# Kernel optimization log

Hardware: AMD Instinct MI355X
Metric: run time of the kernel (lower is better)

The kernel has to match this reference:

```python
import jax, jax.numpy as jnp
import numpy as np

T, B, IN, H = 256, 64, 512, 1024

def setup_inputs() -> dict:
    key = jax.random.key(0)
    ks = jax.random.split(key, 8)
    s_in = 1.0 / np.sqrt(IN)
    s_h = 1.0 / np.sqrt(H)
    return {
        "inp": jax.random.normal(ks[0], (T, B, IN), jnp.float32),
        "img": jax.random.normal(ks[1], (B, H), jnp.float32),
        "Wxh": jax.random.uniform(ks[2], (4 * H, IN), jnp.float32, -s_in, s_in),
        "bxh": jax.random.uniform(ks[3], (4 * H,), jnp.float32, -s_in, s_in),
        "Whh": jax.random.uniform(ks[4], (4 * H, H), jnp.float32, -s_h, s_h),
        "bhh": jax.random.uniform(ks[5], (4 * H,), jnp.float32, -s_h, s_h),
        "Wout": jax.random.uniform(ks[6], (IN, H), jnp.float32, -s_h, s_h),
        "bout": jax.random.uniform(ks[7], (IN,), jnp.float32, -s_h, s_h),
    }

def reference(inp, img, Wxh, bxh, Whh, bhh, Wout, bout):
    t_len, b, _ = inp.shape
    h_dim = Whh.shape[1]
    img4 = jnp.concatenate([img, img, img, img], axis=1)  # [B, 4H]
    # precompute input projection for all timesteps: [T, B, 4H]
    xproj = jnp.einsum('tbi,gi->tbg', inp, Wxh) + bxh
    xproj = xproj.at[0].add(img4)

    def step(carry, xg):
        h, c = carry
        gates = xg + h @ Whh.T + bhh  # [B, 4H]
        i_g, f_g, g_g, o_g = jnp.split(gates, 4, axis=1)
        c = jax.nn.sigmoid(f_g) * c + jax.nn.sigmoid(i_g) * jnp.tanh(g_g)
        h = jax.nn.sigmoid(o_g) * jnp.tanh(c)
        return (h, c), h

    zeros = jnp.zeros((b, h_dim), inp.dtype)
    _, hs = jax.lax.scan(step, (zeros, zeros), xproj)  # hs: [T, B, H]
    out = jnp.einsum('tbh,vh->tbv', hs, Wout) + bout  # [T, B, IN]
    return jax.nn.log_softmax(out, axis=-1)
```

## Files before the change

kernel.cpp:

```cpp
#include <hip/hip_runtime.h>
#include <math.h>

#define T_LEN 256
#define B_SZ  64
#define IN_D  512
#define H_D   1024
#define G4    4096

typedef float  f32x4 __attribute__((ext_vector_type(4)));
typedef short  s16x8 __attribute__((ext_vector_type(8)));
typedef unsigned int u32x4 __attribute__((ext_vector_type(4)));
typedef unsigned short u16;
typedef unsigned int   u32;

__device__ __forceinline__ void gl_lds16(const void* g, void* l) {
  __builtin_amdgcn_global_load_lds(
      (const __attribute__((address_space(1))) unsigned int*)g,
      (__attribute__((address_space(3))) unsigned int*)l, 16, 0, 0);
}

__device__ __forceinline__ u16 f2bf(float f) {
  union { float f; unsigned u; } v; v.f = f;
  unsigned x = v.u;
  unsigned r = (x + 0x7fffu + ((x >> 16) & 1u)) >> 16;
  return (u16)r;
}
__device__ __forceinline__ float bf2f(u16 b) {
  union { unsigned u; float f; } v; v.u = ((unsigned)b) << 16;
  return v.f;
}
__device__ __forceinline__ float sigm(float x) {
  return 1.0f / (1.0f + __expf(-x));
}
__device__ __forceinline__ float tanh_f(float x) {
  float e = __expf(2.0f * x);
  return 1.0f - 2.0f / (e + 1.0f);
}

__global__ void cvt_f32_bf16(const float* __restrict__ src, u16* __restrict__ dst, int n) {
  int i = blockIdx.x * blockDim.x + threadIdx.x;
  int stride = gridDim.x * blockDim.x;
  for (; i < n; i += stride) dst[i] = f2bf(src[i]);
}

__global__ void fill_sentinel(u32* __restrict__ p, int n4) {
  int i = blockIdx.x * blockDim.x + threadIdx.x;
  int stride = gridDim.x * blockDim.x;
  u32x4 s = {0xFFFFFFFFu, 0xFFFFFFFFu, 0xFFFFFFFFu, 0xFFFFFFFFu};
  for (; i < n4; i += stride) {
    u32* dst = p + (size_t)i * 4;
    asm volatile("global_store_dwordx4 %0, %1, off sc1" :: "v"(dst), "v"(s) : "memory");
  }
}

template<int KD, int EPI>
__launch_bounds__(256)
__global__ void gemm_bt(const u16* __restrict__ A, const u16* __restrict__ Bm,
                        const float* __restrict__ bias, const float* __restrict__ img,
                        u16* __restrict__ Cb, float* __restrict__ Cf, int Ncols) {
  __shared__ u16 sA[128 * 64];
  __shared__ u16 sB[128 * 64];
  const int tid  = threadIdx.x;
  const int wave = tid >> 6, lane = tid & 63;
  const int wm = wave >> 1, wn = wave & 1;
  const int mBase = blockIdx.y * 128;
  const int nBase = blockIdx.x * 128;

  f32x4 acc[4][4] = {};

  for (int k0 = 0; k0 < KD; k0 += 64) {
#pragma unroll
    for (int it = 0; it < 4; ++it) {
      int s = it * 256 + tid;
      int row = s >> 3, c = s & 7;
      int gc = c ^ (row & 7);
      const u16* ga = A  + (size_t)(mBase + row) * KD + k0 + gc * 8;
      const u16* gb = Bm + (size_t)(nBase + row) * KD + k0 + gc * 8;
      gl_lds16(ga, &sA[(it * 256 + wave * 64) * 8]);
      gl_lds16(gb, &sB[(it * 256 + wave * 64) * 8]);
    }
    __syncthreads();

    const int q = lane >> 4, rl = lane & 15;
#pragma unroll
    for (int ks = 0; ks < 64; ks += 32) {
      s16x8 af[4], bfr[4];
      int gcb = (ks >> 3) + q;
#pragma unroll
      for (int i = 0; i < 4; ++i) {
        int rowA = wm * 64 + i * 16 + rl;
        af[i]  = *(const s16x8*)&sA[rowA * 64 + (gcb ^ (rowA & 7)) * 8];
        int rowB = wn * 64 + i * 16 + rl;
        bfr[i] = *(const s16x8*)&sB[rowB * 64 + (gcb ^ (rowB & 7)) * 8];
      }
#pragma unroll
      for (int i = 0; i < 4; ++i)
#pragma unroll
        for (int j = 0; j < 4; ++j)
          acc[i][j] = __builtin_amdgcn_mfma_f32_16x16x32_bf16(af[i], bfr[j], acc[i][j], 0, 0, 0);
    }
    __syncthreads();
  }

#pragma unroll
  for (int i = 0; i < 4; ++i) {
    int rbase = mBase + wm * 64 + i * 16 + ((lane >> 4) << 2);
#pragma unroll
    for (int j = 0; j < 4; ++j) {
      int col = nBase + wn * 64 + j * 16 + (lane & 15);
      float bc = bias[col];
#pragma unroll
      for (int r = 0; r < 4; ++r) {
        int row = rbase + r;
        float v = acc[i][j][r] + bc;
        if (EPI == 0) {
          if (row < B_SZ) v += img[row * H_D + (col & (H_D - 1))];
          Cb[(size_t)row * Ncols + col] = f2bf(v);
        } else {
          Cf[(size_t)row * Ncols + col] = v;
        }
      }
    }
  }
}

__launch_bounds__(256, 1)
__global__ void lstm_rec(const u16* __restrict__ WhhB, const u16* __restrict__ xproj,
                         const float* __restrict__ bhh, u32* __restrict__ hs32) {
  __shared__ u16  sH[16 * 1024];
  __shared__ float sGp[2][16][16][17];

  const int tid  = threadIdx.x;
  const int wave = tid >> 6, lane = tid & 63;
  const int grp = blockIdx.x >> 6;
  const int wg  = blockIdx.x & 63;
  const int bBase = grp * 16;
  const int colBase = wg * 16;
  const int q = lane >> 4, rl = lane & 15;

  s16x8 wf[4][8];
  {
    const u16* wb = WhhB + (size_t)(colBase + rl) * H_D + wave * 256 + q * 8;
#pragma unroll
    for (int g = 0; g < 4; ++g)
#pragma unroll
      for (int m = 0; m < 8; ++m)
        wf[g][m] = *(const s16x8*)(wb + (size_t)g * H_D * H_D + m * 32);
  }

  float cst = 0.f;
  const int ub = tid >> 4, uc = tid & 15;
  const int gb = bBase + ub;
  const int gcol = colBase + uc;
  const float bh_i = bhh[0 * H_D + gcol], bh_f = bhh[1 * H_D + gcol];
  const float bh_g = bhh[2 * H_D + gcol], bh_o = bhh[3 * H_D + gcol];

  for (int t = 0; t < T_LEN; ++t) {
    const u16* xp = xproj + ((size_t)t * B_SZ + gb) * G4;
    float gi_ = bf2f(xp[0 * H_D + gcol]) + bh_i;
    float gf_ = bf2f(xp[1 * H_D + gcol]) + bh_f;
    float gg_ = bf2f(xp[2 * H_D + gcol]) + bh_g;
    float go_ = bf2f(xp[3 * H_D + gcol]) + bh_o;

    if (t > 0) {
      u32x4 v[8];
      const u32* hp = hs32 + (size_t)(t - 1) * B_SZ * 512 + (size_t)bBase * 512;
#pragma unroll
      for (int j = 0; j < 8; ++j) {
        int k = j * 64 + lane;
        int row = k >> 5, c = wave * 32 + (k & 31);
        const u32* p = hp + row * 512 + c * 4;
        asm volatile("global_load_dwordx4 %0, %1, off sc1"
                     : "=v"(v[j]) : "v"(p) : "memory");
      }
      asm volatile("s_waitcnt vmcnt(0)" ::: "memory");
      __builtin_amdgcn_sched_barrier(0);
      for (;;) {
        u32 bad = 0;
#pragma unroll
        for (int j = 0; j < 8; ++j) {
          bool st = (v[j][0] == 0xFFFFFFFFu) | (v[j][1] == 0xFFFFFFFFu) |
                    (v[j][2] == 0xFFFFFFFFu) | (v[j][3] == 0xFFFFFFFFu);
          bad |= st ? (1u << j) : 0u;
        }
        if (!__any((int)bad)) break;
#pragma unroll
        for (int j = 0; j < 8; ++j) {
          if (bad & (1u << j)) {
            int k = j * 64 + lane;
            int row = k >> 5, c = wave * 32 + (k & 31);
            const u32* p = hp + row * 512 + c * 4;
            asm volatile("global_load_dwordx4 %0, %1, off sc1"
                         : "=v"(v[j]) : "v"(p) : "memory");
          }
        }
        asm volatile("s_waitcnt vmcnt(0)" ::: "memory");
        __builtin_amdgcn_sched_barrier(0);
      }
#pragma unroll
      for (int j = 0; j < 8; ++j) {
        int k = j * 64 + lane;
        int row = k >> 5, c = wave * 32 + (k & 31);
        *(s16x8*)&sH[row * 1024 + (c ^ (row & 7)) * 8] = *(s16x8*)&v[j];
      }

      f32x4 a0 = {}, a1 = {}, a2 = {}, a3 = {};
#pragma unroll
      for (int m = 0; m < 8; ++m) {
        int chunk = wave * 32 + m * 4 + q;
        s16x8 afr = *(const s16x8*)&sH[rl * 1024 + ((chunk ^ (rl & 7))) * 8];
        a0 = __builtin_amdgcn_mfma_f32_16x16x32_bf16(afr, wf[0][m], a0, 0, 0, 0);
        a1 = __builtin_amdgcn_mfma_f32_16x16x32_bf16(afr, wf[1][m], a1, 0, 0, 0);
        a2 = __builtin_amdgcn_mfma_f32_16x16x32_bf16(afr, wf[2][m], a2, 0, 0, 0);
        a3 = __builtin_amdgcn_mfma_f32_16x16x32_bf16(afr, wf[3][m], a3, 0, 0, 0);
      }
      const int p = t & 1;
#pragma unroll
      for (int r = 0; r < 4; ++r) {
        int row = (lane >> 4) * 4 + r;
        sGp[p][wave * 4 + 0][row][lane & 15] = a0[r];
        sGp[p][wave * 4 + 1][row][lane & 15] = a1[r];
        sGp[p][wave * 4 + 2][row][lane & 15] = a2[r];
        sGp[p][wave * 4 + 3][row][lane & 15] = a3[r];
      }
      __syncthreads();
      gi_ += sGp[p][0][ub][uc] + sGp[p][4][ub][uc] + sGp[p][8][ub][uc]  + sGp[p][12][ub][uc];
      gf_ += sGp[p][1][ub][uc] + sGp[p][5][ub][uc] + sGp[p][9][ub][uc]  + sGp[p][13][ub][uc];
      gg_ += sGp[p][2][ub][uc] + sGp[p][6][ub][uc] + sGp[p][10][ub][uc] + sGp[p][14][ub][uc];
      go_ += sGp[p][3][ub][uc] + sGp[p][7][ub][uc] + sGp[p][11][ub][uc] + sGp[p][15][ub][uc];
    }

    cst = sigm(gf_) * cst + sigm(gi_) * tanh_f(gg_);
    float h = sigm(go_) * tanh_f(cst);

    u32 b = f2bf(h);
    u32 p1 = (u32)__shfl_xor((int)b, 1);
    u32 w0 = b | (p1 << 16);
    u32 w1 = (u32)__shfl_xor((int)w0, 2);
    u32 w2 = (u32)__shfl_xor((int)w0, 4);
    u32 w3 = (u32)__shfl_xor((int)w1, 4);
    if ((tid & 7) == 0) {
      u32x4 pk = {w0, w1, w2, w3};
      u32* dst = hs32 + ((size_t)t * B_SZ + gb) * 512 + (gcol >> 1);
      asm volatile("global_store_dwordx4 %0, %1, off sc1"
                   :: "v"(dst), "v"(pk) : "memory");
    }
  }
  asm volatile("s_waitcnt vmcnt(0)" ::: "memory");
}

__launch_bounds__(256)
__global__ void logsoftmax_rows(float* __restrict__ out) {
  __shared__ float red[8];
  float* p = out + (size_t)blockIdx.x * IN_D;
  const int tid = threadIdx.x;
  float v0 = p[tid], v1 = p[tid + 256];
  float m = fmaxf(v0, v1);
#pragma unroll
  for (int off = 32; off > 0; off >>= 1) m = fmaxf(m, __shfl_down(m, off));
  if ((tid & 63) == 0) red[tid >> 6] = m;
  __syncthreads();
  m = fmaxf(fmaxf(red[0], red[1]), fmaxf(red[2], red[3]));
  float e = __expf(v0 - m) + __expf(v1 - m);
#pragma unroll
  for (int off = 32; off > 0; off >>= 1) e += __shfl_down(e, off);
  if ((tid & 63) == 0) red[4 + (tid >> 6)] = e;
  __syncthreads();
  float ls = m + logf(red[4] + red[5] + red[6] + red[7]);
  p[tid] = v0 - ls;
  p[tid + 256] = v1 - ls;
}

extern "C" void kernel_launch(void* const* d_in, const int* in_sizes, int n_in,
                              void* d_out, int out_size, void* d_ws, size_t ws_size,
                              hipStream_t stream) {
  const float* inp  = (const float*)d_in[0];
  const float* img  = (const float*)d_in[1];
  const float* Wxh  = (const float*)d_in[2];
  const float* bxh  = (const float*)d_in[3];
  const float* Whh  = (const float*)d_in[4];
  const float* bhh  = (const float*)d_in[5];
  const float* Wout = (const float*)d_in[6];
  const float* bout = (const float*)d_in[7];
  float* out = (float*)d_out;

  char* ws = (char*)d_ws;
  u16* inpB   = (u16*)(ws);
  u16* WxhB   = (u16*)(ws + 16777216);
  u16* WhhB   = (u16*)(ws + 20971520);
  u16* WoutB  = (u16*)(ws + 29360128);
  u16* xprojB = (u16*)(ws + 30408704);
  u16* hsB    = (u16*)(ws + 164626432);

  fill_sentinel<<<2048, 256, 0, stream>>>((u32*)hsB, T_LEN * B_SZ * 512 / 4);

  cvt_f32_bf16<<<2048, 256, 0, stream>>>(inp,  inpB,  T_LEN * B_SZ * IN_D);
  cvt_f32_bf16<<<2048, 256, 0, stream>>>(Wxh,  WxhB,  G4 * IN_D);
  cvt_f32_bf16<<<2048, 256, 0, stream>>>(Whh,  WhhB,  G4 * H_D);
  cvt_f32_bf16<<<2048, 256, 0, stream>>>(Wout, WoutB, IN_D * H_D);

  gemm_bt<IN_D, 0><<<dim3(G4 / 128, 16384 / 128), 256, 0, stream>>>(
      inpB, WxhB, bxh, img, xprojB, nullptr, G4);

  lstm_rec<<<256, 256, 0, stream>>>(WhhB, xprojB, bhh, (u32*)hsB);

  gemm_bt<H_D, 1><<<dim3(IN_D / 128, 16384 / 128), 256, 0, stream>>>(
      hsB, WoutB, bout, nullptr, nullptr, out, IN_D);

  logsoftmax_rows<<<16384, 256, 0, stream>>>(out);
}
```

Baseline: 1.021 ms.

## Repartition LSTM recurrence into 128 blocks of 8 waves with full-K per wave

The recurrent kernel now launches 128 blocks of 512 threads, each owning 32 hidden columns for 16 batch rows, instead of 256 blocks of 256 threads owning 16 columns. Each wave now computes one gate and one 16-column half over the full K=1024, so the cross-wave K-split reduction through shared memory is removed. Only four waves poll and load the previous h into LDS, and an extra __syncthreads separates that from the MFMA phase. Halving the block count reduces the number of global producer/consumer participants per step, at the cost of a longer serial MFMA chain per wave and an added barrier.

```diff
diff --git a/kernel.cpp b/kernel.cpp
--- a/kernel.cpp
+++ b/kernel.cpp
@@ -124,32 +124,33 @@
   }
 }
 
-__launch_bounds__(256, 1)
+__launch_bounds__(512, 2)
 __global__ void lstm_rec(const u16* __restrict__ WhhB, const u16* __restrict__ xproj,
                          const float* __restrict__ bhh, u32* __restrict__ hs32) {
   __shared__ u16  sH[16 * 1024];
-  __shared__ float sGp[2][16][16][17];
+  __shared__ float sGp[8][16][17];
 
   const int tid  = threadIdx.x;
   const int wave = tid >> 6, lane = tid & 63;
-  const int grp = blockIdx.x >> 6;
-  const int wg  = blockIdx.x & 63;
+  const int grp = blockIdx.x >> 5;
+  const int slc = blockIdx.x & 31;
   const int bBase = grp * 16;
-  const int colBase = wg * 16;
+  const int colBase = slc * 32;
   const int q = lane >> 4, rl = lane & 15;
-
-  s16x8 wf[4][8];
+  const int cs = wave & 1;
+  const int g  = wave >> 1;
+
+  s16x8 wf[32];
   {
-    const u16* wb = WhhB + (size_t)(colBase + rl) * H_D + wave * 256 + q * 8;
-#pragma unroll
-    for (int g = 0; g < 4; ++g)
-#pragma unroll
-      for (int m = 0; m < 8; ++m)
-        wf[g][m] = *(const s16x8*)(wb + (size_t)g * H_D * H_D + m * 32);
+    const u16* wb = WhhB + (size_t)(g * H_D + colBase + cs * 16 + rl) * H_D + q * 8;
+#pragma unroll
+    for (int m = 0; m < 32; ++m)
+      wf[m] = *(const s16x8*)(wb + m * 32);
   }
 
   float cst = 0.f;
-  const int ub = tid >> 4, uc = tid & 15;
+  const int ub = tid >> 5;
+  const int uc = tid & 31;
   const int gb = bBase + ub;
   const int gcol = colBase + uc;
   const float bh_i = bhh[0 * H_D + gcol], bh_f = bhh[1 * H_D + gcol];
@@ -163,71 +164,68 @@
     float go_ = bf2f(xp[3 * H_D + gcol]) + bh_o;
 
     if (t > 0) {
-      u32x4 v[8];
-      const u32* hp = hs32 + (size_t)(t - 1) * B_SZ * 512 + (size_t)bBase * 512;
-#pragma unroll
-      for (int j = 0; j < 8; ++j) {
-        int k = j * 64 + lane;
-        int row = k >> 5, c = wave * 32 + (k & 31);
-        const u32* p = hp + row * 512 + c * 4;
-        asm volatile("global_load_dwordx4 %0, %1, off sc1"
-                     : "=v"(v[j]) : "v"(p) : "memory");
-      }
-      asm volatile("s_waitcnt vmcnt(0)" ::: "memory");
-      __builtin_amdgcn_sched_barrier(0);
-      for (;;) {
-        u32 bad = 0;
+      if (wave < 4) {
+        u32x4 v[8];
+        const u32* hp = hs32 + (size_t)(t - 1) * B_SZ * 512 + (size_t)bBase * 512;
 #pragma unroll
         for (int j = 0; j < 8; ++j) {
-          bool st = (v[j][0] == 0xFFFFFFFFu) | (v[j][1] == 0xFFFFFFFFu) |
-                    (v[j][2] == 0xFFFFFFFFu) | (v[j][3] == 0xFFFFFFFFu);
-          bad |= st ? (1u << j) : 0u;
-        }
-        if (!__any((int)bad)) break;
-#pragma unroll
-        for (int j = 0; j < 8; ++j) {
-          if (bad & (1u << j)) {
-            int k = j * 64 + lane;
-            int row = k >> 5, c = wave * 32 + (k & 31);
-            const u32* p = hp + row * 512 + c * 4;
-            asm volatile("global_load_dwordx4 %0, %1, off sc1"
-                         : "=v"(v[j]) : "v"(p) : "memory");
-          }
+          int k = j * 64 + lane;
+          int row = k >> 5, c = wave * 32 + (k & 31);
+          const u32* p = hp + row * 512 + c * 4;
+          asm volatile("global_load_dwordx4 %0, %1, off sc1"
+                       : "=v"(v[j]) : "v"(p) : "memory");
         }
         asm volatile("s_waitcnt vmcnt(0)" ::: "memory");
         __builtin_amdgcn_sched_barrier(0);
-      }
-#pragma unroll
-      for (int j = 0; j < 8; ++j) {
-        int k = j * 64 + lane;
-        int row = k >> 5, c = wave * 32 + (k & 31);
-        *(s16x8*)&sH[row * 1024 + (c ^ (row & 7)) * 8] = *(s16x8*)&v[j];
-      }
-
-      f32x4 a0 = {}, a1 = {}, a2 = {}, a3 = {};
-#pragma unroll
-      for (int m = 0; m < 8; ++m) {
-        int chunk = wave * 32 + m * 4 + q;
-        s16x8 afr = *(const s16x8*)&sH[rl * 1024 + ((chunk ^ (rl & 7))) * 8];
-        a0 = __builtin_amdgcn_mfma_f32_16x16x32_bf16(afr, wf[0][m], a0, 0, 0, 0);
-        a1 = __builtin_amdgcn_mfma_f32_16x16x32_bf16(afr, wf[1][m], a1, 0, 0, 0);
-        a2 = __builtin_amdgcn_mfma_f32_16x16x32_bf16(afr, wf[2][m], a2, 0, 0, 0);
-        a3 = __builtin_amdgcn_mfma_f32_16x16x32_bf16(afr, wf[3][m], a3, 0, 0, 0);
-      }
-      const int p = t & 1;
-#pragma unroll
-      for (int r = 0; r < 4; ++r) {
-        int row = (lane >> 4) * 4 + r;
-        sGp[p][wave * 4 + 0][row][lane & 15] = a0[r];
-        sGp[p][wave * 4 + 1][row][lane & 15] = a1[r];
-        sGp[p][wave * 4 + 2][row][lane & 15] = a2[r];
-        sGp[p][wave * 4 + 3][row][lane & 15] = a3[r];
+        for (;;) {
+          u32 bad = 0;
+#pragma unroll
+          for (int j = 0; j < 8; ++j) {
+            bool st = (v[j][0] == 0xFFFFFFFFu) | (v[j][1] == 0xFFFFFFFFu) |
+                      (v[j][2] == 0xFFFFFFFFu) | (v[j][3] == 0xFFFFFFFFu);
+            bad |= st ? (1u << j) : 0u;
+          }
+          if (!__any((int)bad)) break;
+#pragma unroll
+          for (int j = 0; j < 8; ++j) {
+            if (bad & (1u << j)) {
+              int k = j * 64 + lane;
+              int row = k >> 5, c = wave * 32 + (k & 31);
+              const u32* p = hp + row * 512 + c * 4;
+              asm volatile("global_load_dwordx4 %0, %1, off sc1"
+                           : "=v"(v[j]) : "v"(p) : "memory");
+            }
+          }
+          asm volatile("s_waitcnt vmcnt(0)" ::: "memory");
+          __builtin_amdgcn_sched_barrier(0);
+        }
+#pragma unroll
+        for (int j = 0; j < 8; ++j) {
+          int k = j * 64 + lane;
+          int row = k >> 5, c = wave * 32 + (k & 31);
+          *(s16x8*)&sH[row * 1024 + (c ^ (row & 7)) * 8] = *(s16x8*)&v[j];
+        }
       }
       __syncthreads();
-      gi_ += sGp[p][0][ub][uc] + sGp[p][4][ub][uc] + sGp[p][8][ub][uc]  + sGp[p][12][ub][uc];
-      gf_ += sGp[p][1][ub][uc] + sGp[p][5][ub][uc] + sGp[p][9][ub][uc]  + sGp[p][13][ub][uc];
-      gg_ += sGp[p][2][ub][uc] + sGp[p][6][ub][uc] + sGp[p][10][ub][uc] + sGp[p][14][ub][uc];
-      go_ += sGp[p][3][ub][uc] + sGp[p][7][ub][uc] + sGp[p][11][ub][uc] + sGp[p][15][ub][uc];
+
+      f32x4 a = {};
+#pragma unroll
+      for (int m = 0; m < 32; ++m) {
+        int c = m * 4 + q;
+        s16x8 afr = *(const s16x8*)&sH[rl * 1024 + ((c ^ (rl & 7))) * 8];
+        a = __builtin_amdgcn_mfma_f32_16x16x32_bf16(afr, wf[m], a, 0, 0, 0);
+      }
+#pragma unroll
+      for (int r = 0; r < 4; ++r)
+        sGp[g * 2 + cs][(lane >> 4) * 4 + r][lane & 15] = a[r];
+      __syncthreads();
+      {
+        const int cc = uc >> 4, lc = uc & 15;
+        gi_ += sGp[0 * 2 + cc][ub][lc];
+        gf_ += sGp[1 * 2 + cc][ub][lc];
+        gg_ += sGp[2 * 2 + cc][ub][lc];
+        go_ += sGp[3 * 2 + cc][ub][lc];
+      }
     }
 
     cst = sigm(gf_) * cst + sigm(gi_) * tanh_f(gg_);
@@ -302,7 +300,7 @@
   gemm_bt<IN_D, 0><<<dim3(G4 / 128, 16384 / 128), 256, 0, stream>>>(
       inpB, WxhB, bxh, img, xprojB, nullptr, G4);
 
-  lstm_rec<<<256, 256, 0, stream>>>(WhhB, xprojB, bhh, (u32*)hsB);
+  lstm_rec<<<128, 512, 0, stream>>>(WhhB, xprojB, bhh, (u32*)hsB);
 
   gemm_bt<H_D, 1><<<dim3(IN_D / 128, 16384 / 128), 256, 0, stream>>>(
       hsB, WoutB, bout, nullptr, nullptr, out, IN_D);
```

After: 1.097 ms. 7.4% more time.
